# Optimization experiments

Measured on AMD Instinct MI355X. Metric: run time of the kernel, lower is better.

## Reference

```python
import jax, jax.numpy as jnp
import numpy as np

D_IN = 1024
D_OUT = 1024
NUM_HEADS = 16
HEAD_DIM = D_OUT // NUM_HEADS


def setup_inputs() -> dict:
    key = jax.random.key(0)
    ks = jax.random.split(key, 6)
    s = 0.02
    x = jax.random.normal(ks[0], (4, 2048, D_IN), dtype=jnp.float32)
    # nn.Linear weights are [out, in]
    Wq = jax.random.normal(ks[1], (D_OUT, D_IN), dtype=jnp.float32) * s
    Wk = jax.random.normal(ks[2], (D_OUT, D_IN), dtype=jnp.float32) * s
    Wv = jax.random.normal(ks[3], (D_OUT, D_IN), dtype=jnp.float32) * s
    Wo = jax.random.normal(ks[4], (D_OUT, D_OUT), dtype=jnp.float32) * s
    bo = jax.random.normal(ks[5], (D_OUT,), dtype=jnp.float32) * s
    return {"x": x, "Wq": Wq, "Wk": Wk, "Wv": Wv, "Wo": Wo, "bo": bo}


def reference(x, Wq, Wk, Wv, Wo, bo):
    B, T, _ = x.shape
    # project and split heads: [B, H, T, hd]
    def proj(W):
        return (x @ W.T).reshape(B, T, NUM_HEADS, HEAD_DIM).transpose(0, 2, 1, 3)
    q, k, v = proj(Wq), proj(Wk), proj(Wv)
    scores = jnp.einsum('bhqd,bhkd->bhqk', q, k) / jnp.sqrt(jnp.float32(HEAD_DIM))
    causal = jnp.tril(jnp.ones((T, T), dtype=bool))  # True = keep
    scores = jnp.where(causal, scores, -jnp.inf)
    attn = jax.nn.softmax(scores, axis=-1)
    ctx = jnp.einsum('bhqk,bhkd->bhqd', attn, v)  # [B,H,T,hd]
    ctx = ctx.transpose(0, 2, 1, 3).reshape(B, T, D_OUT)
    return ctx @ Wo.T + bo
```

## Files before the change

### kernel.cpp

```cpp
#include <hip/hip_runtime.h>

#define NH 16
#define HD 64
#define TSEQ 2048
#define DMODEL 1024

typedef __attribute__((ext_vector_type(8))) short short8;
typedef __attribute__((ext_vector_type(4))) float f32x4;

static __device__ __forceinline__ unsigned short f2bf(float f) {
    unsigned u = __builtin_bit_cast(unsigned, f);
    u += 0x7FFF + ((u >> 16) & 1);
    return (unsigned short)(u >> 16);
}

static __device__ __forceinline__ unsigned cvtpk(float a, float b) {
    unsigned r;
    asm("v_cvt_pk_bf16_f32 %0, %1, %2" : "=v"(r) : "v"(a), "v"(b));
    return r;
}

__global__ __launch_bounds__(256) void cast_f32_bf16(const float* __restrict__ src,
                                                     unsigned short* __restrict__ dst, int n4) {
    int i = blockIdx.x * 256 + threadIdx.x;
    if (i >= n4) return;
    float4 v = reinterpret_cast<const float4*>(src)[i];
    ushort4 o;
    o.x = f2bf(v.x); o.y = f2bf(v.y); o.z = f2bf(v.z); o.w = f2bf(v.w);
    reinterpret_cast<ushort4*>(dst)[i] = o;
}

__global__ __launch_bounds__(256) void cast_weights(const float* __restrict__ Wq,
                                                    const float* __restrict__ Wk,
                                                    const float* __restrict__ Wv,
                                                    const float* __restrict__ Wo,
                                                    unsigned short* __restrict__ dq,
                                                    unsigned short* __restrict__ dk,
                                                    unsigned short* __restrict__ dv,
                                                    unsigned short* __restrict__ dwo) {
    int g = blockIdx.x >> 10;
    int i = (blockIdx.x & 1023) * 256 + threadIdx.x;
    const float* s = (g == 0) ? Wq : (g == 1) ? Wk : (g == 2) ? Wv : Wo;
    unsigned short* d = (g == 0) ? dq : (g == 1) ? dk : (g == 2) ? dv : dwo;
    float4 v = reinterpret_cast<const float4*>(s)[i];
    ushort4 o;
    o.x = f2bf(v.x); o.y = f2bf(v.y); o.z = f2bf(v.z); o.w = f2bf(v.w);
    reinterpret_cast<ushort4*>(d)[i] = o;
}

static __device__ __forceinline__ void gemm256_mainloop(
    const unsigned short* __restrict__ A, const unsigned short* __restrict__ Bt,
    int m0, int n0, unsigned short* As, unsigned short* Bs, f32x4 acc[8][2]) {
    const int tid = threadIdx.x, lane = tid & 63, w = tid >> 6;
    const int wr = w >> 2, wc = w & 3;
    const int lg = lane >> 4, ll = lane & 15;
    const int srow = tid >> 3;
    const int scol8 = (tid & 7) * 8;

    const f32x4 zero = {0.f, 0.f, 0.f, 0.f};
#pragma unroll
    for (int i = 0; i < 8; i++)
#pragma unroll
        for (int j = 0; j < 2; j++) acc[i][j] = zero;

    auto stageA2 = [&](int kt, int buf, int h) {
#pragma unroll
        for (int s = h * 2; s < h * 2 + 2; ++s) {
            int row = s * 64 + srow;
            int csw = scol8 ^ (((row >> 2) & 1) << 4);
            __builtin_amdgcn_global_load_lds(
                (const __attribute__((address_space(1))) void*)(A + (size_t)(m0 + row) * DMODEL + kt * 64 + csw),
                (__attribute__((address_space(3))) void*)(As + buf * 16384 + s * 4096 + w * 512), 16, 0, 0);
        }
    };
    auto stageB1 = [&](int kt, int buf, int s) {
        int row = s * 64 + srow;
        int csw = scol8 ^ (((row >> 2) & 1) << 4);
        __builtin_amdgcn_global_load_lds(
            (const __attribute__((address_space(1))) void*)(Bt + (size_t)(n0 + row) * DMODEL + kt * 64 + csw),
            (__attribute__((address_space(3))) void*)(Bs + buf * 8192 + s * 4096 + w * 512), 16, 0, 0);
    };
    auto ldA = [&](int buf, int row, int ks) -> short8 {
        int col = (ks * 32 + lg * 8) ^ (((row >> 2) & 1) << 4);
        return *(const short8*)(As + buf * 16384 + row * 64 + col);
    };
    auto ldB = [&](int buf, int row, int ks) -> short8 {
        int col = (ks * 32 + lg * 8) ^ (((row >> 2) & 1) << 4);
        return *(const short8*)(Bs + buf * 8192 + row * 64 + col);
    };

    stageA2(0, 0, 0); stageA2(0, 0, 1);
    stageB1(0, 0, 0); stageB1(0, 0, 1);
    stageB1(1, 1, 0); stageB1(1, 1, 1);
    asm volatile("s_waitcnt vmcnt(2)" ::: "memory");
    __builtin_amdgcn_s_barrier();
    __builtin_amdgcn_sched_barrier(0);

#pragma unroll 1
    for (int kt = 0; kt < 16; ++kt) {
        const int pa = kt & 1;
        const int pb = kt % 3;
        short8 bfr[2][2];
        short8 afr[2][2];

#pragma unroll
        for (int j = 0; j < 2; j++)
#pragma unroll
            for (int ks = 0; ks < 2; ks++)
                bfr[j][ks] = ldB(pb, wc * 32 + j * 16 + ll, ks);
#pragma unroll
        for (int i2 = 0; i2 < 2; i2++)
#pragma unroll
            for (int ks = 0; ks < 2; ks++)
                afr[i2][ks] = ldA(pa, wr * 128 + i2 * 16 + ll, ks);
        if (kt + 1 < 16) stageA2(kt + 1, pa ^ 1, 0);
        __builtin_amdgcn_s_barrier();
        __builtin_amdgcn_sched_barrier(0);
        __builtin_amdgcn_s_setprio(1);
#pragma unroll
        for (int i2 = 0; i2 < 2; i2++)
#pragma unroll
            for (int j = 0; j < 2; j++) {
                acc[i2][j] = __builtin_amdgcn_mfma_f32_16x16x32_bf16(afr[i2][0], bfr[j][0], acc[i2][j], 0, 0, 0);
                acc[i2][j] = __builtin_amdgcn_mfma_f32_16x16x32_bf16(afr[i2][1], bfr[j][1], acc[i2][j], 0, 0, 0);
            }
        __builtin_amdgcn_s_setprio(0);
        __builtin_amdgcn_s_barrier();
        __builtin_amdgcn_sched_barrier(0);

#pragma unroll
        for (int i2 = 0; i2 < 2; i2++)
#pragma unroll
            for (int ks = 0; ks < 2; ks++)
                afr[i2][ks] = ldA(pa, wr * 128 + (2 + i2) * 16 + ll, ks);
        if (kt + 1 < 16) stageA2(kt + 1, pa ^ 1, 1);
        __builtin_amdgcn_s_barrier();
        __builtin_amdgcn_sched_barrier(0);
        __builtin_amdgcn_s_setprio(1);
#pragma unroll
        for (int i2 = 0; i2 < 2; i2++)
#pragma unroll
            for (int j = 0; j < 2; j++) {
                acc[2 + i2][j] = __builtin_amdgcn_mfma_f32_16x16x32_bf16(afr[i2][0], bfr[j][0], acc[2 + i2][j], 0, 0, 0);
                acc[2 + i2][j] = __builtin_amdgcn_mfma_f32_16x16x32_bf16(afr[i2][1], bfr[j][1], acc[2 + i2][j], 0, 0, 0);
            }
        __builtin_amdgcn_s_setprio(0);
        __builtin_amdgcn_s_barrier();
        __builtin_amdgcn_sched_barrier(0);

#pragma unroll
        for (int i2 = 0; i2 < 2; i2++)
#pragma unroll
            for (int ks = 0; ks < 2; ks++)
                afr[i2][ks] = ldA(pa, wr * 128 + (4 + i2) * 16 + ll, ks);
        if (kt + 2 < 16) stageB1(kt + 2, (kt + 2) % 3, 0);
        __builtin_amdgcn_s_barrier();
        __builtin_amdgcn_sched_barrier(0);
        __builtin_amdgcn_s_setprio(1);
#pragma unroll
        for (int i2 = 0; i2 < 2; i2++)
#pragma unroll
            for (int j = 0; j < 2; j++) {
                acc[4 + i2][j] = __builtin_amdgcn_mfma_f32_16x16x32_bf16(afr[i2][0], bfr[j][0], acc[4 + i2][j], 0, 0, 0);
                acc[4 + i2][j] = __builtin_amdgcn_mfma_f32_16x16x32_bf16(afr[i2][1], bfr[j][1], acc[4 + i2][j], 0, 0, 0);
            }
        __builtin_amdgcn_s_setprio(0);
        __builtin_amdgcn_s_barrier();
        __builtin_amdgcn_sched_barrier(0);

#pragma unroll
        for (int i2 = 0; i2 < 2; i2++)
#pragma unroll
            for (int ks = 0; ks < 2; ks++)
                afr[i2][ks] = ldA(pa, wr * 128 + (6 + i2) * 16 + ll, ks);
        if (kt + 2 < 16) {
            stageB1(kt + 2, (kt + 2) % 3, 1);
            asm volatile("s_waitcnt vmcnt(2)" ::: "memory");
        } else {
            asm volatile("s_waitcnt vmcnt(0)" ::: "memory");
        }
        __builtin_amdgcn_s_barrier();
        __builtin_amdgcn_sched_barrier(0);
        __builtin_amdgcn_s_setprio(1);
#pragma unroll
        for (int i2 = 0; i2 < 2; i2++)
#pragma unroll
            for (int j = 0; j < 2; j++) {
                acc[6 + i2][j] = __builtin_amdgcn_mfma_f32_16x16x32_bf16(afr[i2][0], bfr[j][0], acc[6 + i2][j], 0, 0, 0);
                acc[6 + i2][j] = __builtin_amdgcn_mfma_f32_16x16x32_bf16(afr[i2][1], bfr[j][1], acc[6 + i2][j], 0, 0, 0);
            }
        __builtin_amdgcn_s_setprio(0);
        __builtin_amdgcn_s_barrier();
        __builtin_amdgcn_sched_barrier(0);
    }
}

#define QSCALE 0.180336880f
__global__ __launch_bounds__(512) void gemm_qkv(const unsigned short* __restrict__ xb,
                                                const unsigned short* __restrict__ Wqb,
                                                const unsigned short* __restrict__ Wkb,
                                                const unsigned short* __restrict__ Wvb,
                                                unsigned short* __restrict__ Q,
                                                unsigned short* __restrict__ K,
                                                unsigned short* __restrict__ Vt) {
    __shared__ __attribute__((aligned(16))) unsigned short As[2 * 256 * 64];
    __shared__ __attribute__((aligned(16))) unsigned short Bs[3 * 128 * 64];
    const int m0 = blockIdx.x * 256;
    const int n0 = blockIdx.y * 128;
    const int z = blockIdx.z;
    const unsigned short* Bt = (z == 0) ? Wqb : ((z == 1) ? Wkb : Wvb);
    unsigned short* out = (z == 0) ? Q : ((z == 1) ? K : Vt);

    f32x4 acc[8][2];
    gemm256_mainloop(xb, Bt, m0, n0, As, Bs, acc);

    const int lane = threadIdx.x & 63, w = threadIdx.x >> 6;
    const int wr = w >> 2, wc = w & 3;
    const int lg = lane >> 4, ll = lane & 15;
    const float sc = (z == 0) ? QSCALE : 1.0f;
#pragma unroll
    for (int i = 0; i < 8; i++)
#pragma unroll
        for (int j = 0; j < 2; j++)
#pragma unroll
            for (int r = 0; r < 4; r++) {
                int row = m0 + wr * 128 + i * 16 + lg * 4 + r;
                int col = n0 + wc * 32 + j * 16 + ll;
                int b = row >> 11, t = row & 2047;
                int h = col >> 6, d = col & 63;
                unsigned short v = f2bf(acc[i][j][r] * sc);
                if (z == 2)
                    out[(((size_t)(b * NH + h)) * HD + d) * TSEQ + t] = v;
                else
                    out[(((size_t)(b * NH + h)) * TSEQ + t) * HD + d] = v;
            }
}

__global__ __launch_bounds__(512) void gemm_out(const unsigned short* __restrict__ ctx,
                                                const unsigned short* __restrict__ Wob,
                                                const float* __restrict__ bo,
                                                float* __restrict__ out) {
    __shared__ __attribute__((aligned(16))) unsigned short As[2 * 256 * 64];
    __shared__ __attribute__((aligned(16))) unsigned short Bs[3 * 128 * 64];
    const int m0 = blockIdx.x * 256;
    const int n0 = blockIdx.y * 128;

    f32x4 acc[8][2];
    gemm256_mainloop(ctx, Wob, m0, n0, As, Bs, acc);

    const int lane = threadIdx.x & 63, w = threadIdx.x >> 6;
    const int wr = w >> 2, wc = w & 3;
    const int lg = lane >> 4, ll = lane & 15;
#pragma unroll
    for (int i = 0; i < 8; i++)
#pragma unroll
        for (int j = 0; j < 2; j++) {
            int col = n0 + wc * 32 + j * 16 + ll;
            float bias = bo[col];
#pragma unroll
            for (int r = 0; r < 4; r++) {
                int row = m0 + wr * 128 + i * 16 + lg * 4 + r;
                out[(size_t)row * DMODEL + col] = acc[i][j][r] + bias;
            }
        }
}

__global__ __launch_bounds__(256) void attn(const unsigned short* __restrict__ Qg,
                                            const unsigned short* __restrict__ Kg,
                                            const unsigned short* __restrict__ Vg,
                                            unsigned short* __restrict__ ctx) {
    __shared__ __attribute__((aligned(16))) unsigned short Ks[64][72];
    __shared__ __attribute__((aligned(16))) unsigned short Vs[64][72];
    __shared__ __attribute__((aligned(16))) unsigned short Pl[128][76];

    const int tid = threadIdx.x, lane = tid & 63, w = tid >> 6;
    const int wq = w * 32;
    const int lg = lane >> 4;
    const int ll = lane & 15;
    const int bh = blockIdx.x;
    const int q0 = (gridDim.y - 1 - blockIdx.y) * 128;
    const unsigned short* Qh = Qg + (size_t)bh * TSEQ * HD;
    const unsigned short* Kh = Kg + (size_t)bh * TSEQ * HD;
    const unsigned short* Vh = Vg + (size_t)bh * HD * TSEQ;

    short8 qf[2][2];
#pragma unroll
    for (int rb = 0; rb < 2; rb++)
#pragma unroll
        for (int ks = 0; ks < 2; ks++)
            qf[rb][ks] = *(const short8*)(Qh + (size_t)(q0 + wq + rb * 16 + ll) * HD + ks * 32 + lg * 8);

    float mrun[2] = {-1e30f, -1e30f}, lrun[2] = {0.f, 0.f};
    const f32x4 zerov = {0.f, 0.f, 0.f, 0.f};
    f32x4 o_t[2][4];
#pragma unroll
    for (int rb = 0; rb < 2; rb++)
#pragma unroll
        for (int db = 0; db < 4; db++) o_t[rb][db] = zerov;

    const int sr = tid >> 3;
    const int sc = (tid & 7) * 8;
    short8 kreg0, kreg1, vreg0, vreg1;
    {
        kreg0 = *(const short8*)(Kh + (size_t)(sr) * HD + sc);
        kreg1 = *(const short8*)(Kh + (size_t)(sr + 32) * HD + sc);
        vreg0 = *(const short8*)(Vh + (size_t)sr * TSEQ + sc);
        vreg1 = *(const short8*)(Vh + (size_t)(sr + 32) * TSEQ + sc);
    }

    const int nkv = q0 / 64 + 2;
    for (int kt = 0; kt < nkv; kt++) {
        const int kv0 = kt * 64;
        __builtin_amdgcn_s_barrier();
        __builtin_amdgcn_sched_barrier(0);
        *(short8*)&Ks[sr][sc] = kreg0;
        *(short8*)&Ks[sr + 32][sc] = kreg1;
        *(short8*)&Vs[sr][sc] = vreg0;
        *(short8*)&Vs[sr + 32][sc] = vreg1;
        if (kt + 1 < nkv) {
            const int nv0 = kv0 + 64;
            kreg0 = *(const short8*)(Kh + (size_t)(nv0 + sr) * HD + sc);
            kreg1 = *(const short8*)(Kh + (size_t)(nv0 + sr + 32) * HD + sc);
            vreg0 = *(const short8*)(Vh + (size_t)sr * TSEQ + nv0 + sc);
            vreg1 = *(const short8*)(Vh + (size_t)(sr + 32) * TSEQ + nv0 + sc);
        }
        __builtin_amdgcn_sched_barrier(0);
        asm volatile("s_waitcnt lgkmcnt(0)" ::: "memory");
        __builtin_amdgcn_s_barrier();
        __builtin_amdgcn_sched_barrier(0);

        short8 af0[4], af1[4];
#pragma unroll
        for (int cb = 0; cb < 4; cb++) {
            af0[cb] = *(const short8*)&Ks[cb * 16 + ll][lg * 8];
            af1[cb] = *(const short8*)&Ks[cb * 16 + ll][32 + lg * 8];
        }
        f32x4 st[2][4];
#pragma unroll
        for (int rb = 0; rb < 2; rb++)
#pragma unroll
            for (int cb = 0; cb < 4; cb++)
                st[rb][cb] = __builtin_amdgcn_mfma_f32_16x16x32_bf16(af0[cb], qf[rb][0], zerov, 0, 0, 0);
#pragma unroll
        for (int rb = 0; rb < 2; rb++)
#pragma unroll
            for (int cb = 0; cb < 4; cb++)
                st[rb][cb] = __builtin_amdgcn_mfma_f32_16x16x32_bf16(af1[cb], qf[rb][1], st[rb][cb], 0, 0, 0);

        if (kv0 + 63 > q0) {
#pragma unroll
            for (int rb = 0; rb < 2; rb++)
#pragma unroll
                for (int cb = 0; cb < 4; cb++)
#pragma unroll
                    for (int r = 0; r < 4; r++) {
                        int kvl = cb * 16 + lg * 4 + r;
                        int ql = wq + rb * 16 + ll;
                        if (kv0 + kvl > q0 + ql) st[rb][cb][r] = -1e30f;
                    }
        }

        float mx[2];
#pragma unroll
        for (int rb = 0; rb < 2; rb++) {
            float a0 = fmaxf(fmaxf(st[rb][0][0], st[rb][0][1]), fmaxf(st[rb][0][2], st[rb][0][3]));
            float a1 = fmaxf(fmaxf(st[rb][1][0], st[rb][1][1]), fmaxf(st[rb][1][2], st[rb][1][3]));
            float a2 = fmaxf(fmaxf(st[rb][2][0], st[rb][2][1]), fmaxf(st[rb][2][2], st[rb][2][3]));
            float a3 = fmaxf(fmaxf(st[rb][3][0], st[rb][3][1]), fmaxf(st[rb][3][2], st[rb][3][3]));
            float m = fmaxf(fmaxf(a0, a1), fmaxf(a2, a3));
            m = fmaxf(m, __shfl_xor(m, 16));
            m = fmaxf(m, __shfl_xor(m, 32));
            mx[rb] = m;
        }
        float need = fmaxf(mx[0] - mrun[0], mx[1] - mrun[1]);
        if (__any(need > 8.f)) {
#pragma unroll
            for (int rb = 0; rb < 2; rb++) {
                float mold = mrun[rb];
                float mn = fmaxf(mold, mx[rb]);
                float rs = __builtin_amdgcn_exp2f(mold - mn);
                mrun[rb] = mn;
                lrun[rb] *= rs;
#pragma unroll
                for (int db = 0; db < 4; db++)
#pragma unroll
                    for (int r = 0; r < 4; r++) o_t[rb][db][r] *= rs;
            }
        }
#pragma unroll
        for (int rb = 0; rb < 2; rb++) {
            float sum = 0.f;
#pragma unroll
            for (int cb = 0; cb < 4; cb++) {
                float p0 = __builtin_amdgcn_exp2f(st[rb][cb][0] - mrun[rb]);
                float p1 = __builtin_amdgcn_exp2f(st[rb][cb][1] - mrun[rb]);
                float p2 = __builtin_amdgcn_exp2f(st[rb][cb][2] - mrun[rb]);
                float p3 = __builtin_amdgcn_exp2f(st[rb][cb][3] - mrun[rb]);
                sum += (p0 + p1) + (p2 + p3);
                uint2 pw;
                pw.x = cvtpk(p0, p1);
                pw.y = cvtpk(p2, p3);
                *(uint2*)&Pl[wq + rb * 16 + ll][cb * 16 + lg * 4] = pw;
            }
            sum += __shfl_xor(sum, 16);
            sum += __shfl_xor(sum, 32);
            lrun[rb] += sum;
        }
        asm volatile("s_waitcnt lgkmcnt(0)" ::: "memory");
        __builtin_amdgcn_sched_barrier(0);

#pragma unroll
        for (int ks = 0; ks < 2; ks++) {
            short8 pa[2], va[4];
#pragma unroll
            for (int rb = 0; rb < 2; rb++)
                pa[rb] = *(const short8*)&Pl[wq + rb * 16 + ll][ks * 32 + lg * 8];
#pragma unroll
            for (int db = 0; db < 4; db++)
                va[db] = *(const short8*)&Vs[db * 16 + ll][ks * 32 + lg * 8];
#pragma unroll
            for (int rb = 0; rb < 2; rb++)
#pragma unroll
                for (int db = 0; db < 4; db++)
                    o_t[rb][db] = __builtin_amdgcn_mfma_f32_16x16x32_bf16(va[db], pa[rb], o_t[rb][db], 0, 0, 0);
        }
    }

    const int b = bh >> 4, h = bh & 15;
#pragma unroll
    for (int rb = 0; rb < 2; rb++) {
        float linv = 1.f / lrun[rb];
#pragma unroll
        for (int db = 0; db < 4; db++) {
            uint2 pw;
            pw.x = cvtpk(o_t[rb][db][0] * linv, o_t[rb][db][1] * linv);
            pw.y = cvtpk(o_t[rb][db][2] * linv, o_t[rb][db][3] * linv);
            *(uint2*)&Pl[wq + rb * 16 + ll][db * 16 + lg * 4] = pw;
        }
    }
    asm volatile("s_waitcnt lgkmcnt(0)" ::: "memory");
    __builtin_amdgcn_sched_barrier(0);
#pragma unroll
    for (int rb = 0; rb < 2; rb++)
#pragma unroll
        for (int half = 0; half < 2; half++) {
            short8 v = *(const short8*)&Pl[wq + rb * 16 + ll][half * 32 + lg * 8];
            size_t row = (size_t)(b * TSEQ + q0 + wq + rb * 16 + ll);
            *(short8*)(ctx + (row * NH + h) * HD + half * 32 + lg * 8) = v;
        }
}

extern "C" void kernel_launch(void* const* d_in, const int* in_sizes, int n_in,
                              void* d_out, int out_size, void* d_ws, size_t ws_size,
                              hipStream_t stream) {
    const float* x  = (const float*)d_in[0];
    const float* Wq = (const float*)d_in[1];
    const float* Wk = (const float*)d_in[2];
    const float* Wv = (const float*)d_in[3];
    const float* Wo = (const float*)d_in[4];
    const float* bo = (const float*)d_in[5];
    float* out = (float*)d_out;

    char* ws = (char*)d_ws;
    unsigned short* xb   = (unsigned short*)(ws);
    unsigned short* Wqb  = (unsigned short*)(ws + 16777216);
    unsigned short* Wkb  = (unsigned short*)(ws + 18874368);
    unsigned short* Wvb  = (unsigned short*)(ws + 20971520);
    unsigned short* Wob  = (unsigned short*)(ws + 23068672);
    unsigned short* Qb   = (unsigned short*)(ws + 25165824);
    unsigned short* Kb   = (unsigned short*)(ws + 41943040);
    unsigned short* Vtb  = (unsigned short*)(ws + 58720256);
    unsigned short* ctxb = (unsigned short*)(ws + 75497472);

    cast_f32_bf16<<<8192, 256, 0, stream>>>(x, xb, 2097152);
    cast_weights<<<4096, 256, 0, stream>>>(Wq, Wk, Wv, Wo, Wqb, Wkb, Wvb, Wob);

    gemm_qkv<<<dim3(32, 8, 3), 512, 0, stream>>>(xb, Wqb, Wkb, Wvb, Qb, Kb, Vtb);
    attn<<<dim3(64, 16), 256, 0, stream>>>(Qb, Kb, Vtb, ctxb);
    gemm_out<<<dim3(32, 8), 512, 0, stream>>>(ctxb, Wob, bo, out);
}
```

Baseline: 207.8 us.

## Reshape GEMM warp tiling to 4x2 warps with 64x64 subtiles and XOR swizzle

Changes the 8-warp GEMM mainloop from a 2x4 warp grid with 128x32 warp tiles to a 4x2 grid with 64x64 warp tiles, and processes the K dimension in two halves of 16 MFMAs each. It replaces four barrier-separated phases with two per K step. It also swaps the LDS swizzle for an 8-way XOR on row bits to cut bank conflicts. The square warp tiles need fewer LDS fragment loads per MFMA and fewer barriers, at the cost of a different prefetch cadence for the A and B stages.

```diff
diff --git a/kernel.cpp b/kernel.cpp
--- a/kernel.cpp
+++ b/kernel.cpp
@@ -50,48 +50,41 @@
 
 static __device__ __forceinline__ void gemm256_mainloop(
     const unsigned short* __restrict__ A, const unsigned short* __restrict__ Bt,
-    int m0, int n0, unsigned short* As, unsigned short* Bs, f32x4 acc[8][2]) {
+    int m0, int n0, unsigned short* As, unsigned short* Bs, f32x4 acc[4][4]) {
     const int tid = threadIdx.x, lane = tid & 63, w = tid >> 6;
-    const int wr = w >> 2, wc = w & 3;
+    const int wr = w >> 1, wc = w & 1;
     const int lg = lane >> 4, ll = lane & 15;
-    const int srow = tid >> 3;
-    const int scol8 = (tid & 7) * 8;
+    const int strow = tid >> 3;
+    const int csw = ((tid & 7) * 8) ^ ((strow & 7) << 3);
+    const int axor = (ll & 7) << 3;
 
     const f32x4 zero = {0.f, 0.f, 0.f, 0.f};
 #pragma unroll
-    for (int i = 0; i < 8; i++)
-#pragma unroll
-        for (int j = 0; j < 2; j++) acc[i][j] = zero;
-
-    auto stageA2 = [&](int kt, int buf, int h) {
-#pragma unroll
-        for (int s = h * 2; s < h * 2 + 2; ++s) {
-            int row = s * 64 + srow;
-            int csw = scol8 ^ (((row >> 2) & 1) << 4);
+    for (int i = 0; i < 4; i++)
+#pragma unroll
+        for (int j = 0; j < 4; j++) acc[i][j] = zero;
+
+    auto stageA = [&](int kt, int buf, int half) {
+#pragma unroll
+        for (int s = half * 2; s < half * 2 + 2; ++s) {
+            int row = s * 64 + strow;
             __builtin_amdgcn_global_load_lds(
                 (const __attribute__((address_space(1))) void*)(A + (size_t)(m0 + row) * DMODEL + kt * 64 + csw),
                 (__attribute__((address_space(3))) void*)(As + buf * 16384 + s * 4096 + w * 512), 16, 0, 0);
         }
     };
-    auto stageB1 = [&](int kt, int buf, int s) {
-        int row = s * 64 + srow;
-        int csw = scol8 ^ (((row >> 2) & 1) << 4);
-        __builtin_amdgcn_global_load_lds(
-            (const __attribute__((address_space(1))) void*)(Bt + (size_t)(n0 + row) * DMODEL + kt * 64 + csw),
-            (__attribute__((address_space(3))) void*)(Bs + buf * 8192 + s * 4096 + w * 512), 16, 0, 0);
+    auto stageB = [&](int kt, int buf) {
+#pragma unroll
+        for (int s = 0; s < 2; ++s) {
+            int row = s * 64 + strow;
+            __builtin_amdgcn_global_load_lds(
+                (const __attribute__((address_space(1))) void*)(Bt + (size_t)(n0 + row) * DMODEL + kt * 64 + csw),
+                (__attribute__((address_space(3))) void*)(Bs + buf * 8192 + s * 4096 + w * 512), 16, 0, 0);
+        }
     };
-    auto ldA = [&](int buf, int row, int ks) -> short8 {
-        int col = (ks * 32 + lg * 8) ^ (((row >> 2) & 1) << 4);
-        return *(const short8*)(As + buf * 16384 + row * 64 + col);
-    };
-    auto ldB = [&](int buf, int row, int ks) -> short8 {
-        int col = (ks * 32 + lg * 8) ^ (((row >> 2) & 1) << 4);
-        return *(const short8*)(Bs + buf * 8192 + row * 64 + col);
-    };
-
-    stageA2(0, 0, 0); stageA2(0, 0, 1);
-    stageB1(0, 0, 0); stageB1(0, 0, 1);
-    stageB1(1, 1, 0); stageB1(1, 1, 1);
+
+    stageA(0, 0, 0); stageA(0, 0, 1);
+    stageB(0, 0); stageB(1, 1);
     asm volatile("s_waitcnt vmcnt(2)" ::: "memory");
     __builtin_amdgcn_s_barrier();
     __builtin_amdgcn_sched_barrier(0);
@@ -100,98 +93,56 @@
     for (int kt = 0; kt < 16; ++kt) {
         const int pa = kt & 1;
         const int pb = kt % 3;
-        short8 bfr[2][2];
-        short8 afr[2][2];
-
-#pragma unroll
-        for (int j = 0; j < 2; j++)
-#pragma unroll
-            for (int ks = 0; ks < 2; ks++)
-                bfr[j][ks] = ldB(pb, wc * 32 + j * 16 + ll, ks);
-#pragma unroll
-        for (int i2 = 0; i2 < 2; i2++)
-#pragma unroll
-            for (int ks = 0; ks < 2; ks++)
-                afr[i2][ks] = ldA(pa, wr * 128 + i2 * 16 + ll, ks);
-        if (kt + 1 < 16) stageA2(kt + 1, pa ^ 1, 0);
-        __builtin_amdgcn_s_barrier();
-        __builtin_amdgcn_sched_barrier(0);
-        __builtin_amdgcn_s_setprio(1);
-#pragma unroll
-        for (int i2 = 0; i2 < 2; i2++)
-#pragma unroll
-            for (int j = 0; j < 2; j++) {
-                acc[i2][j] = __builtin_amdgcn_mfma_f32_16x16x32_bf16(afr[i2][0], bfr[j][0], acc[i2][j], 0, 0, 0);
-                acc[i2][j] = __builtin_amdgcn_mfma_f32_16x16x32_bf16(afr[i2][1], bfr[j][1], acc[i2][j], 0, 0, 0);
+
+        {
+            short8 af[4], bf[4];
+#pragma unroll
+            for (int i = 0; i < 4; i++)
+                af[i] = *(const short8*)(As + pa * 16384 + (wr * 64 + i * 16 + ll) * 64 + ((lg * 8) ^ axor));
+#pragma unroll
+            for (int j = 0; j < 4; j++)
+                bf[j] = *(const short8*)(Bs + pb * 8192 + (wc * 64 + j * 16 + ll) * 64 + ((lg * 8) ^ axor));
+            if (kt + 1 < 16) stageA(kt + 1, pa ^ 1, 0);
+            __builtin_amdgcn_s_barrier();
+            __builtin_amdgcn_sched_barrier(0);
+            __builtin_amdgcn_s_setprio(1);
+#pragma unroll
+            for (int i = 0; i < 4; i++)
+#pragma unroll
+                for (int j = 0; j < 4; j++)
+                    acc[i][j] = __builtin_amdgcn_mfma_f32_16x16x32_bf16(af[i], bf[j], acc[i][j], 0, 0, 0);
+            __builtin_amdgcn_s_setprio(0);
+            __builtin_amdgcn_s_barrier();
+            __builtin_amdgcn_sched_barrier(0);
+        }
+
+        {
+            short8 af[4], bf[4];
+#pragma unroll
+            for (int i = 0; i < 4; i++)
+                af[i] = *(const short8*)(As + pa * 16384 + (wr * 64 + i * 16 + ll) * 64 + ((32 + lg * 8) ^ axor));
+#pragma unroll
+            for (int j = 0; j < 4; j++)
+                bf[j] = *(const short8*)(Bs + pb * 8192 + (wc * 64 + j * 16 + ll) * 64 + ((32 + lg * 8) ^ axor));
+            if (kt + 1 < 16) stageA(kt + 1, pa ^ 1, 1);
+            if (kt + 2 < 16) {
+                stageB(kt + 2, (kt + 2) % 3);
+                asm volatile("s_waitcnt vmcnt(2)" ::: "memory");
+            } else {
+                asm volatile("s_waitcnt vmcnt(0)" ::: "memory");
             }
-        __builtin_amdgcn_s_setprio(0);
-        __builtin_amdgcn_s_barrier();
-        __builtin_amdgcn_sched_barrier(0);
-
-#pragma unroll
-        for (int i2 = 0; i2 < 2; i2++)
-#pragma unroll
-            for (int ks = 0; ks < 2; ks++)
-                afr[i2][ks] = ldA(pa, wr * 128 + (2 + i2) * 16 + ll, ks);
-        if (kt + 1 < 16) stageA2(kt + 1, pa ^ 1, 1);
-        __builtin_amdgcn_s_barrier();
-        __builtin_amdgcn_sched_barrier(0);
-        __builtin_amdgcn_s_setprio(1);
-#pragma unroll
-        for (int i2 = 0; i2 < 2; i2++)
-#pragma unroll
-            for (int j = 0; j < 2; j++) {
-                acc[2 + i2][j] = __builtin_amdgcn_mfma_f32_16x16x32_bf16(afr[i2][0], bfr[j][0], acc[2 + i2][j], 0, 0, 0);
-                acc[2 + i2][j] = __builtin_amdgcn_mfma_f32_16x16x32_bf16(afr[i2][1], bfr[j][1], acc[2 + i2][j], 0, 0, 0);
-            }
-        __builtin_amdgcn_s_setprio(0);
-        __builtin_amdgcn_s_barrier();
-        __builtin_amdgcn_sched_barrier(0);
-
-#pragma unroll
-        for (int i2 = 0; i2 < 2; i2++)
-#pragma unroll
-            for (int ks = 0; ks < 2; ks++)
-                afr[i2][ks] = ldA(pa, wr * 128 + (4 + i2) * 16 + ll, ks);
-        if (kt + 2 < 16) stageB1(kt + 2, (kt + 2) % 3, 0);
-        __builtin_amdgcn_s_barrier();
-        __builtin_amdgcn_sched_barrier(0);
-        __builtin_amdgcn_s_setprio(1);
-#pragma unroll
-        for (int i2 = 0; i2 < 2; i2++)
-#pragma unroll
-            for (int j = 0; j < 2; j++) {
-                acc[4 + i2][j] = __builtin_amdgcn_mfma_f32_16x16x32_bf16(afr[i2][0], bfr[j][0], acc[4 + i2][j], 0, 0, 0);
-                acc[4 + i2][j] = __builtin_amdgcn_mfma_f32_16x16x32_bf16(afr[i2][1], bfr[j][1], acc[4 + i2][j], 0, 0, 0);
-            }
-        __builtin_amdgcn_s_setprio(0);
-        __builtin_amdgcn_s_barrier();
-        __builtin_amdgcn_sched_barrier(0);
-
-#pragma unroll
-        for (int i2 = 0; i2 < 2; i2++)
-#pragma unroll
-            for (int ks = 0; ks < 2; ks++)
-                afr[i2][ks] = ldA(pa, wr * 128 + (6 + i2) * 16 + ll, ks);
-        if (kt + 2 < 16) {
-            stageB1(kt + 2, (kt + 2) % 3, 1);
-            asm volatile("s_waitcnt vmcnt(2)" ::: "memory");
-        } else {
-            asm volatile("s_waitcnt vmcnt(0)" ::: "memory");
-        }
-        __builtin_amdgcn_s_barrier();
-        __builtin_amdgcn_sched_barrier(0);
-        __builtin_amdgcn_s_setprio(1);
-#pragma unroll
-        for (int i2 = 0; i2 < 2; i2++)
-#pragma unroll
-            for (int j = 0; j < 2; j++) {
-                acc[6 + i2][j] = __builtin_amdgcn_mfma_f32_16x16x32_bf16(afr[i2][0], bfr[j][0], acc[6 + i2][j], 0, 0, 0);
-                acc[6 + i2][j] = __builtin_amdgcn_mfma_f32_16x16x32_bf16(afr[i2][1], bfr[j][1], acc[6 + i2][j], 0, 0, 0);
-            }
-        __builtin_amdgcn_s_setprio(0);
-        __builtin_amdgcn_s_barrier();
-        __builtin_amdgcn_sched_barrier(0);
+            __builtin_amdgcn_s_barrier();
+            __builtin_amdgcn_sched_barrier(0);
+            __builtin_amdgcn_s_setprio(1);
+#pragma unroll
+            for (int i = 0; i < 4; i++)
+#pragma unroll
+                for (int j = 0; j < 4; j++)
+                    acc[i][j] = __builtin_amdgcn_mfma_f32_16x16x32_bf16(af[i], bf[j], acc[i][j], 0, 0, 0);
+            __builtin_amdgcn_s_setprio(0);
+            __builtin_amdgcn_s_barrier();
+            __builtin_amdgcn_sched_barrier(0);
+        }
     }
 }
 
@@ -211,21 +162,21 @@
     const unsigned short* Bt = (z == 0) ? Wqb : ((z == 1) ? Wkb : Wvb);
     unsigned short* out = (z == 0) ? Q : ((z == 1) ? K : Vt);
 
-    f32x4 acc[8][2];
+    f32x4 acc[4][4];
     gemm256_mainloop(xb, Bt, m0, n0, As, Bs, acc);
 
     const int lane = threadIdx.x & 63, w = threadIdx.x >> 6;
-    const int wr = w >> 2, wc = w & 3;
+    const int wr = w >> 1, wc = w & 1;
     const int lg = lane >> 4, ll = lane & 15;
     const float sc = (z == 0) ? QSCALE : 1.0f;
 #pragma unroll
-    for (int i = 0; i < 8; i++)
-#pragma unroll
-        for (int j = 0; j < 2; j++)
+    for (int i = 0; i < 4; i++)
+#pragma unroll
+        for (int j = 0; j < 4; j++)
 #pragma unroll
             for (int r = 0; r < 4; r++) {
-                int row = m0 + wr * 128 + i * 16 + lg * 4 + r;
-                int col = n0 + wc * 32 + j * 16 + ll;
+                int row = m0 + wr * 64 + i * 16 + lg * 4 + r;
+                int col = n0 + wc * 64 + j * 16 + ll;
                 int b = row >> 11, t = row & 2047;
                 int h = col >> 6, d = col & 63;
                 unsigned short v = f2bf(acc[i][j][r] * sc);
@@ -245,21 +196,21 @@
     const int m0 = blockIdx.x * 256;
     const int n0 = blockIdx.y * 128;
 
-    f32x4 acc[8][2];
+    f32x4 acc[4][4];
     gemm256_mainloop(ctx, Wob, m0, n0, As, Bs, acc);
 
     const int lane = threadIdx.x & 63, w = threadIdx.x >> 6;
-    const int wr = w >> 2, wc = w & 3;
+    const int wr = w >> 1, wc = w & 1;
     const int lg = lane >> 4, ll = lane & 15;
 #pragma unroll
-    for (int i = 0; i < 8; i++)
-#pragma unroll
-        for (int j = 0; j < 2; j++) {
-            int col = n0 + wc * 32 + j * 16 + ll;
+    for (int i = 0; i < 4; i++)
+#pragma unroll
+        for (int j = 0; j < 4; j++) {
+            int col = n0 + wc * 64 + j * 16 + ll;
             float bias = bo[col];
 #pragma unroll
             for (int r = 0; r < 4; r++) {
-                int row = m0 + wr * 128 + i * 16 + lg * 4 + r;
+                int row = m0 + wr * 64 + i * 16 + lg * 4 + r;
                 out[(size_t)row * DMODEL + col] = acc[i][j][r] + bias;
             }
         }
```

Measured after the change: 200.0 us. -3.7%, faster.
